# Kernel optimization log

Hardware: AMD Instinct MI355X
Metric: run time of the kernel (lower is better)

The kernel has to match this reference:

```python
import jax, jax.numpy as jnp
import numpy as np

N_NODES = 100000
N_EDGES = 1600000
IN_FEATS = 128
N_HIDDEN = 32
N_CLASSES = 47
HEADS = (4, 4)
NEG_SLOPE = 0.2


def setup_inputs() -> dict:
    key = jax.random.key(0)
    ks = jax.random.split(key, 12)
    x = jax.random.normal(ks[0], (N_NODES, IN_FEATS), dtype=jnp.float32)
    src = jax.random.randint(ks[1], (N_EDGES,), 0, N_NODES)
    dst = jax.random.randint(ks[2], (N_EDGES,), 0, N_NODES)
    inverse_idx = jax.random.randint(ks[3], (N_NODES,), 0, N_NODES)
    h1 = HEADS[0] * N_HIDDEN
    s1 = 1.0 / np.sqrt(IN_FEATS)
    W1 = jax.random.normal(ks[4], (IN_FEATS, h1), dtype=jnp.float32) * s1
    al1 = jax.random.normal(ks[5], (HEADS[0], N_HIDDEN), dtype=jnp.float32) * 0.1
    ar1 = jax.random.normal(ks[6], (HEADS[0], N_HIDDEN), dtype=jnp.float32) * 0.1
    b1 = jnp.zeros((h1,), dtype=jnp.float32)
    h2 = HEADS[1] * N_CLASSES
    s2 = 1.0 / np.sqrt(h1)
    W2 = jax.random.normal(ks[7], (h1, h2), dtype=jnp.float32) * s2
    al2 = jax.random.normal(ks[8], (HEADS[1], N_CLASSES), dtype=jnp.float32) * 0.1
    ar2 = jax.random.normal(ks[9], (HEADS[1], N_CLASSES), dtype=jnp.float32) * 0.1
    b2 = jnp.zeros((h2,), dtype=jnp.float32)
    return {"x": x, "src": src, "dst": dst, "inverse_idx": inverse_idx,
            "W1": W1, "al1": al1, "ar1": ar1, "b1": b1,
            "W2": W2, "al2": al2, "ar2": ar2, "b2": b2}


def gat_conv(h, src, dst, W, al, ar, b, heads, out_dim, apply_elu):
    # DGL GATConv (feat_drop=attn_drop=0, eval mode):
    # projected per-head features, edge attention, per-dst softmax, aggregate.
    feat = (h @ W).reshape(-1, heads, out_dim)               # (N, H, D)
    el = jnp.einsum('nhd,hd->nh', feat, al)                  # (N, H)
    er = jnp.einsum('nhd,hd->nh', feat, ar)                  # (N, H)
    e = el[src] + er[dst]                                    # (E, H)
    e = jnp.where(e > 0, e, NEG_SLOPE * e)                   # LeakyReLU
    m = jax.ops.segment_max(e, dst, num_segments=N_NODES)    # (N, H)
    m = jnp.where(jnp.isfinite(m), m, 0.0)
    ex = jnp.exp(e - m[dst])
    s = jax.ops.segment_sum(ex, dst, num_segments=N_NODES)   # (N, H)
    alpha = ex / jnp.maximum(s[dst], 1e-9)                   # (E, H)
    msg = feat[src] * alpha[:, :, None]                      # (E, H, D)
    out = jax.ops.segment_sum(msg, dst, num_segments=N_NODES)  # (N, H, D)
    out = out + b.reshape(1, heads, out_dim)
    if apply_elu:
        out = jax.nn.elu(out)
    return out


def reference(x, src, dst, inverse_idx, W1, al1, ar1, b1, W2, al2, ar2, b2):
    # Layer 0: GATConv + ELU, flatten heads, then NPFeatureShuffle reindex.
    h = gat_conv(x, src, dst, W1, al1, ar1, b1, HEADS[0], N_HIDDEN, True)
    h = h.reshape(N_NODES, HEADS[0] * N_HIDDEN)
    h = h[inverse_idx]  # cross-partition shuffle reindex
    # Layer 1: GATConv, no activation, mean over heads.
    h = gat_conv(h, src, dst, W2, al2, ar2, b2, HEADS[1], N_CLASSES, False)
    return h.mean(axis=1)  # (N, n_classes)
```

## Files before the change

### kernel.cpp

```cpp
#include <hip/hip_runtime.h>
#include <hip/hip_bf16.h>
#include <hip/hip_fp16.h>
#include <type_traits>

#define N_NODES 100000
#define N_EDGES 1600000

typedef _Float16 half8_t __attribute__((ext_vector_type(8)));
typedef _Float16 half4_t __attribute__((ext_vector_type(4)));
typedef float floatx4 __attribute__((ext_vector_type(4)));

__global__ void count_deg(const int* __restrict__ dst, int* __restrict__ deg, int E) {
    int i = blockIdx.x * blockDim.x + threadIdx.x;
    if (i < E) atomicAdd(&deg[dst[i]], 1);
}

__global__ void block_sums(const int* __restrict__ deg, int* __restrict__ bsum, int N) {
    __shared__ int ws[4];
    const int t = threadIdx.x;
    int i = blockIdx.x * 256 + t;
    int v = (i < N) ? deg[i] : 0;
    #pragma unroll
    for (int o = 32; o; o >>= 1) v += __shfl_down(v, o, 64);
    if ((t & 63) == 0) ws[t >> 6] = v;
    __syncthreads();
    if (t == 0) bsum[blockIdx.x] = ws[0] + ws[1] + ws[2] + ws[3];
}

__global__ void scan_bsum(int* __restrict__ bsum, int nb) {
    __shared__ int sh[512];
    const int t = threadIdx.x;
    sh[t] = (t < nb) ? bsum[t] : 0;
    __syncthreads();
    for (int o = 1; o < 512; o <<= 1) {
        int v = (t >= o) ? sh[t - o] : 0;
        __syncthreads();
        sh[t] += v;
        __syncthreads();
    }
    if (t < nb) bsum[t] = sh[t];
}

__global__ void scan_final(const int* __restrict__ deg, const int* __restrict__ bsum,
                           int* __restrict__ row_ptr, int* __restrict__ cursor,
                           int* __restrict__ csr_dst, int N) {
    __shared__ int ws[4];
    const int t = threadIdx.x;
    const int b = blockIdx.x;
    const int i = b * 256 + t;
    const int lane = t & 63;
    const int wid = t >> 6;
    int v = (i < N) ? deg[i] : 0;
    int x = v;
    #pragma unroll
    for (int o = 1; o < 64; o <<= 1) {
        int y = __shfl_up(x, o, 64);
        if (lane >= o) x += y;
    }
    if (lane == 63) ws[wid] = x;
    __syncthreads();
    int prefix = (b > 0) ? bsum[b - 1] : 0;
    for (int k = 0; k < wid; ++k) prefix += ws[k];
    if (i < N) {
        int st = prefix + x - v;
        row_ptr[i + 1] = prefix + x;
        cursor[i] = st;
        for (int j = 0; j < v; ++j) csr_dst[st + j] = i;
    }
    if (i == 0) row_ptr[0] = 0;
}

__global__ void scatter_edges_part(const int* __restrict__ src, const int* __restrict__ dst,
                                   int* __restrict__ cursor, int* __restrict__ e_src, int E) {
    const int part = blockIdx.x & 7;
    const int sb = blockIdx.x >> 3;
    const int nslices = gridDim.x >> 3;
    const int psz = N_NODES / 8;
    const int lo = part * psz;
    const int hi = (part == 7) ? N_NODES : lo + psz;
    const int begin = (int)((long long)E * sb / nslices);
    const int end = (int)((long long)E * (sb + 1) / nslices);
    for (int i = begin + threadIdx.x; i < end; i += blockDim.x) {
        int d = dst[i];
        if (d >= lo && d < hi) {
            int p = atomicAdd(&cursor[d], 1);
            e_src[p] = src[i];
        }
    }
}

__global__ void prep_w(const float* __restrict__ W1, const float* __restrict__ W2,
                       __half* __restrict__ Wt1, __half* __restrict__ Wt2) {
    const int c = blockIdx.x;
    const int k = threadIdx.x;
    if (c < 128) {
        Wt1[c * 128 + k] = __float2half(W1[k * 128 + c]);
    } else {
        int c2 = c - 128;
        float v = (c2 < 188) ? W2[k * 188 + c2] : 0.f;
        Wt2[c2 * 128 + k] = __float2half(v);
    }
}

template <int NTILES, int NLOG, int OSTRIDE, bool PADSTORE, bool GATHER, typename AT>
__global__ __launch_bounds__(256) void gemm_mfma(
    const AT* __restrict__ A, const __half* __restrict__ Wt,
    __half* __restrict__ C, const int* __restrict__ gather, int N) {
    constexpr int LDA = 136;
    __shared__ _Float16 As[64 * LDA];
    __shared__ int ridx[64];
    const int tid = threadIdx.x;
    const int r0 = blockIdx.x * 64;

    if (tid < 64) {
        int row = r0 + tid;
        int pr = 0;
        if (row < N) pr = GATHER ? gather[row] : row;
        ridx[tid] = pr;
    }
    __syncthreads();

    {
        const int r = tid >> 2, q = tid & 3;
        const int src = ridx[r];
        if constexpr (std::is_same<AT, float>::value) {
            const float4* A4 = (const float4*)A;
            #pragma unroll
            for (int i = 0; i < 8; ++i) {
                float4 v = A4[(size_t)src * 32 + q * 8 + i];
                half4_t hv = {(_Float16)v.x, (_Float16)v.y, (_Float16)v.z, (_Float16)v.w};
                *(half4_t*)&As[r * LDA + q * 32 + i * 4] = hv;
            }
        } else {
            const uint4* A4 = (const uint4*)A;
            #pragma unroll
            for (int i = 0; i < 4; ++i) {
                uint4 v = A4[(size_t)src * 16 + q * 4 + i];
                *(uint4*)&As[r * LDA + q * 32 + i * 8] = v;
            }
        }
    }
    __syncthreads();

    const int lane = tid & 63;
    const int wave = tid >> 6;
    const int col = lane & 15;
    const int quad = lane >> 4;
    const int arow = wave * 16 + col;

    floatx4 acc[NTILES];
    #pragma unroll
    for (int t = 0; t < NTILES; ++t) acc[t] = (floatx4){0.f, 0.f, 0.f, 0.f};

    #pragma unroll
    for (int kc = 0; kc < 4; ++kc) {
        half8_t a = *(const half8_t*)&As[arow * LDA + kc * 32 + quad * 8];
        #pragma unroll
        for (int t = 0; t < NTILES; ++t) {
            half8_t b = *(const half8_t*)&Wt[(size_t)(t * 16 + col) * 128 + kc * 32 + quad * 8];
            acc[t] = __builtin_amdgcn_mfma_f32_16x16x32_f16(a, b, acc[t], 0, 0, 0);
        }
    }

    #pragma unroll
    for (int t = 0; t < NTILES; ++t) {
        #pragma unroll
        for (int r = 0; r < 4; ++r) {
            int row = r0 + wave * 16 + quad * 4 + r;
            int c = t * 16 + col;
            if (row < N && c < NLOG) {
                int sc = PADSTORE ? (c + c / 47) : c;
                C[(size_t)row * OSTRIDE + sc] = __float2half(acc[t][r]);
            }
        }
    }
}

__global__ __launch_bounds__(256) void elr1_wave(
    const __half* __restrict__ feat, const float* __restrict__ al, const float* __restrict__ ar,
    float* __restrict__ el, float* __restrict__ er) {
    const int t = threadIdx.x;
    const int lane = t & 63;
    const int n = blockIdx.x * 4 + (t >> 6);
    const __half2* f2 = (const __half2*)feat;
    float2 g = __half22float2(f2[(size_t)n * 64 + lane]);
    float2 a = ((const float2*)al)[lane];
    float2 b = ((const float2*)ar)[lane];
    float sl = g.x * a.x + g.y * a.y;
    float sr = g.x * b.x + g.y * b.y;
    #pragma unroll
    for (int o = 1; o < 16; o <<= 1) {
        sl += __shfl_xor(sl, o, 64);
        sr += __shfl_xor(sr, o, 64);
    }
    if ((lane & 15) == 0) {
        int h = lane >> 4;
        el[n * 4 + h] = sl;
        er[n * 4 + h] = sr;
    }
}

__global__ __launch_bounds__(256) void elr2_wave(
    const __half* __restrict__ feat, const float* __restrict__ al, const float* __restrict__ ar,
    float* __restrict__ el, float* __restrict__ er) {
    const int t = threadIdx.x;
    const int lane = t & 63;
    const int n = blockIdx.x * 4 + (t >> 6);
    float sl = 0.f, sr = 0.f;
    int h = 0, q = 0;
    if (lane < 48) {
        h = lane / 12;
        q = lane - h * 12;
        const half4_t* f4 = (const half4_t*)feat;
        half4_t g = f4[(size_t)n * 48 + lane];
        const int d0 = q * 4;
        #pragma unroll
        for (int j = 0; j < 4; ++j) {
            int d = d0 + j;
            if (d < 47) {
                float gv = (float)g[j];
                sl = fmaf(gv, al[h * 47 + d], sl);
                sr = fmaf(gv, ar[h * 47 + d], sr);
            }
        }
    }
    sl += __shfl(sl, lane + 6, 64);
    sr += __shfl(sr, lane + 6, 64);
    sl += __shfl(sl, lane + 3, 64);
    sr += __shfl(sr, lane + 3, 64);
    float l1 = __shfl(sl, lane + 1, 64), l2 = __shfl(sl, lane + 2, 64);
    float r1 = __shfl(sr, lane + 1, 64), r2 = __shfl(sr, lane + 2, 64);
    sl += l1 + l2;
    sr += r1 + r2;
    if (lane < 48 && q == 0) {
        el[n * 4 + h] = sl;
        er[n * 4 + h] = sr;
    }
}

__global__ void edge_weights(const int* __restrict__ e_src, const int* __restrict__ csr_dst,
                             const float* __restrict__ el, const float* __restrict__ er,
                             __half* __restrict__ w, int E) {
    int i = blockIdx.x * blockDim.x + threadIdx.x;
    if (i >= E) return;
    int s = e_src[i], d = csr_dst[i];
    float4 a = ((const float4*)el)[s];
    float4 b = ((const float4*)er)[d];
    float e0 = a.x + b.x; e0 = (e0 > 0.f) ? e0 : 0.2f * e0;
    float e1 = a.y + b.y; e1 = (e1 > 0.f) ? e1 : 0.2f * e1;
    float e2 = a.z + b.z; e2 = (e2 > 0.f) ? e2 : 0.2f * e2;
    float e3 = a.w + b.w; e3 = (e3 > 0.f) ? e3 : 0.2f * e3;
    __half2* w2 = (__half2*)w;
    w2[i * 2 + 0] = __floats2half2_rn(__expf(e0), __expf(e1));
    w2[i * 2 + 1] = __floats2half2_rn(__expf(e2), __expf(e3));
}

__global__ __launch_bounds__(256) void gat_gather1(
    const __half* __restrict__ feat, const __half* __restrict__ w,
    const int* __restrict__ row_ptr, const int* __restrict__ e_src,
    const float* __restrict__ bias, __half* __restrict__ out) {
    const int t = threadIdx.x;
    const int lane = t & 63;
    const int n = blockIdx.x * 4 + (t >> 6);
    const int h = lane >> 4;
    const int start = row_ptr[n], end = row_ptr[n + 1];
    const __half2* f2 = (const __half2*)feat;
    float ax = 0.f, ay = 0.f, s = 0.f;
    int i = start;
    for (; i + 4 <= end; i += 4) {
        int sv0 = e_src[i + 0], sv1 = e_src[i + 1], sv2 = e_src[i + 2], sv3 = e_src[i + 3];
        float w0 = __half2float(w[(i + 0) * 4 + h]);
        float w1 = __half2float(w[(i + 1) * 4 + h]);
        float w2 = __half2float(w[(i + 2) * 4 + h]);
        float w3 = __half2float(w[(i + 3) * 4 + h]);
        __half2 f0 = f2[(size_t)sv0 * 64 + lane];
        __half2 f1 = f2[(size_t)sv1 * 64 + lane];
        __half2 f2v = f2[(size_t)sv2 * 64 + lane];
        __half2 f3 = f2[(size_t)sv3 * 64 + lane];
        float2 g0 = __half22float2(f0), g1 = __half22float2(f1);
        float2 g2 = __half22float2(f2v), g3 = __half22float2(f3);
        s += (w0 + w1) + (w2 + w3);
        ax += w0 * g0.x + w1 * g1.x + w2 * g2.x + w3 * g3.x;
        ay += w0 * g0.y + w1 * g1.y + w2 * g2.y + w3 * g3.y;
    }
    for (; i < end; ++i) {
        int sv = e_src[i];
        float ww = __half2float(w[i * 4 + h]);
        float2 g = __half22float2(f2[(size_t)sv * 64 + lane]);
        s += ww;
        ax += ww * g.x;
        ay += ww * g.y;
    }
    float inv = 1.f / fmaxf(s, 1e-9f);
    float ox = ax * inv + bias[lane * 2 + 0];
    float oy = ay * inv + bias[lane * 2 + 1];
    ox = (ox > 0.f) ? ox : (__expf(ox) - 1.f);
    oy = (oy > 0.f) ? oy : (__expf(oy) - 1.f);
    ((__half2*)out)[(size_t)n * 64 + lane] = __floats2half2_rn(ox, oy);
}

__global__ __launch_bounds__(256) void gat_gather2(
    const __half* __restrict__ feat, const __half* __restrict__ w,
    const int* __restrict__ row_ptr, const int* __restrict__ e_src,
    const float* __restrict__ bias, float* __restrict__ out) {
    const int t = threadIdx.x;
    const int lane = t & 63;
    const int n = blockIdx.x * 4 + (t >> 6);
    if (lane < 48) {
        const int h = lane / 12;
        const int q = lane - h * 12;
        const int start = row_ptr[n], end = row_ptr[n + 1];
        const half4_t* f4 = (const half4_t*)feat;
        float a0 = 0.f, a1 = 0.f, a2 = 0.f, a3 = 0.f, s = 0.f;
        int i = start;
        for (; i + 4 <= end; i += 4) {
            int sv0 = e_src[i + 0], sv1 = e_src[i + 1], sv2 = e_src[i + 2], sv3 = e_src[i + 3];
            float w0 = __half2float(w[(i + 0) * 4 + h]);
            float w1 = __half2float(w[(i + 1) * 4 + h]);
            float w2 = __half2float(w[(i + 2) * 4 + h]);
            float w3 = __half2float(w[(i + 3) * 4 + h]);
            half4_t f0 = f4[(size_t)sv0 * 48 + lane];
            half4_t f1 = f4[(size_t)sv1 * 48 + lane];
            half4_t f2 = f4[(size_t)sv2 * 48 + lane];
            half4_t f3 = f4[(size_t)sv3 * 48 + lane];
            s += (w0 + w1) + (w2 + w3);
            a0 += w0 * (float)f0[0] + w1 * (float)f1[0] + w2 * (float)f2[0] + w3 * (float)f3[0];
            a1 += w0 * (float)f0[1] + w1 * (float)f1[1] + w2 * (float)f2[1] + w3 * (float)f3[1];
            a2 += w0 * (float)f0[2] + w1 * (float)f1[2] + w2 * (float)f2[2] + w3 * (float)f3[2];
            a3 += w0 * (float)f0[3] + w1 * (float)f1[3] + w2 * (float)f2[3] + w3 * (float)f3[3];
        }
        for (; i < end; ++i) {
            int sv = e_src[i];
            float ww = __half2float(w[i * 4 + h]);
            half4_t f0 = f4[(size_t)sv * 48 + lane];
            s += ww;
            a0 += ww * (float)f0[0];
            a1 += ww * (float)f0[1];
            a2 += ww * (float)f0[2];
            a3 += ww * (float)f0[3];
        }
        if (q == 11) a3 = 0.f;
        float inv = 1.f / fmaxf(s, 1e-9f);
        const int d0 = q * 4;
        float b0 = bias[h * 47 + d0 + 0];
        float b1 = bias[h * 47 + d0 + 1];
        float b2 = bias[h * 47 + d0 + 2];
        float b3 = (d0 + 3 < 47) ? bias[h * 47 + d0 + 3] : 0.f;
        float r0 = a0 * inv + b0;
        float r1 = a1 * inv + b1;
        float r2 = a2 * inv + b2;
        float r3 = a3 * inv + b3;
        float t0 = r0 + __shfl(r0, lane + 12, 64) + __shfl(r0, lane + 24, 64) + __shfl(r0, lane + 36, 64);
        float t1 = r1 + __shfl(r1, lane + 12, 64) + __shfl(r1, lane + 24, 64) + __shfl(r1, lane + 36, 64);
        float t2 = r2 + __shfl(r2, lane + 12, 64) + __shfl(r2, lane + 24, 64) + __shfl(r2, lane + 36, 64);
        float t3 = r3 + __shfl(r3, lane + 12, 64) + __shfl(r3, lane + 24, 64) + __shfl(r3, lane + 36, 64);
        if (h == 0) {
            size_t base = (size_t)n * 47 + d0;
            out[base + 0] = 0.25f * t0;
            out[base + 1] = 0.25f * t1;
            out[base + 2] = 0.25f * t2;
            if (d0 + 3 < 47) out[base + 3] = 0.25f * t3;
        }
    }
}

extern "C" void kernel_launch(void* const* d_in, const int* in_sizes, int n_in,
                              void* d_out, int out_size, void* d_ws, size_t ws_size,
                              hipStream_t stream) {
    const int N = N_NODES, E = N_EDGES;
    const float* x    = (const float*)d_in[0];
    const int*   src  = (const int*)d_in[1];
    const int*   dst  = (const int*)d_in[2];
    const int*   inv  = (const int*)d_in[3];
    const float* W1   = (const float*)d_in[4];
    const float* al1  = (const float*)d_in[5];
    const float* ar1  = (const float*)d_in[6];
    const float* b1   = (const float*)d_in[7];
    const float* W2   = (const float*)d_in[8];
    const float* al2  = (const float*)d_in[9];
    const float* ar2  = (const float*)d_in[10];
    const float* b2   = (const float*)d_in[11];
    float* out = (float*)d_out;

    char* p = (char*)d_ws;
    auto carve = [&](size_t bytes) {
        char* q = p;
        p += (bytes + 255) & ~size_t(255);
        return q;
    };
    __half* feat1   = (__half*)carve((size_t)N * 128 * 2);
    __half* feat2   = (__half*)carve((size_t)N * 192 * 2);
    __half* hbuf    = (__half*)carve((size_t)N * 128 * 2);
    __half* Wt1     = (__half*)carve(128 * 128 * 2);
    __half* Wt2     = (__half*)carve(192 * 128 * 2);
    float*  el      = (float*)carve((size_t)N * 4 * 4);
    float*  er      = (float*)carve((size_t)N * 4 * 4);
    int*    deg     = (int*)carve((size_t)N * 4);
    int*    row_ptr = (int*)carve((size_t)(N + 1) * 4);
    int*    cursor  = (int*)carve((size_t)N * 4);
    int*    bsum    = (int*)carve(512 * 4);
    int*    e_src   = (int*)carve((size_t)E * 4);
    int*    csr_dst = (int*)carve((size_t)E * 4);
    __half* ew      = (__half*)carve((size_t)E * 4 * 2);

    const int nb = (N + 255) / 256;

    hipMemsetAsync(deg, 0, (size_t)N * 4, stream);
    count_deg<<<(E + 255) / 256, 256, 0, stream>>>(dst, deg, E);
    block_sums<<<nb, 256, 0, stream>>>(deg, bsum, N);
    scan_bsum<<<1, 512, 0, stream>>>(bsum, nb);
    scan_final<<<nb, 256, 0, stream>>>(deg, bsum, row_ptr, cursor, csr_dst, N);
    scatter_edges_part<<<2048, 256, 0, stream>>>(src, dst, cursor, e_src, E);

    prep_w<<<320, 128, 0, stream>>>(W1, W2, Wt1, Wt2);

    gemm_mfma<8, 128, 128, false, false, float><<<(N + 63) / 64, 256, 0, stream>>>(x, Wt1, feat1, nullptr, N);
    elr1_wave<<<(N + 3) / 4, 256, 0, stream>>>(feat1, al1, ar1, el, er);
    edge_weights<<<(E + 255) / 256, 256, 0, stream>>>(e_src, csr_dst, el, er, ew, E);
    gat_gather1<<<(N + 3) / 4, 256, 0, stream>>>(feat1, ew, row_ptr, e_src, b1, hbuf);

    gemm_mfma<12, 188, 192, true, true, __half><<<(N + 63) / 64, 256, 0, stream>>>(hbuf, Wt2, feat2, inv, N);
    elr2_wave<<<(N + 3) / 4, 256, 0, stream>>>(feat2, al2, ar2, el, er);
    edge_weights<<<(E + 255) / 256, 256, 0, stream>>>(e_src, csr_dst, el, er, ew, E);
    gat_gather2<<<(N + 3) / 4, 256, 0, stream>>>(feat2, ew, row_ptr, e_src, b2, out);
}
```

Before: 581.6 us.

## Fold attention vectors into GEMM weights and compute edge weights inside gather

Precomputes W·al and W·ar as extra weight columns so the GEMM emits el/er directly, removing the separate elr kernels. Edge softmax numerators are now computed on the fly in the gather kernels from el[src]+er[dst], eliminating the edge_weights kernels, the ew buffer and the csr_dst array along with its serial fill loop in scan_final. This removes several launches and about 1.6M-edge-sized reads and writes per layer, at the cost of an extra random el load plus exp per edge per lane in the gathers and slightly different rounding because el/er now come from fp16-rounded folded weights.

```diff
diff --git a/kernel.cpp b/kernel.cpp
--- a/kernel.cpp
+++ b/kernel.cpp
@@ -42,8 +42,7 @@
 }
 
 __global__ void scan_final(const int* __restrict__ deg, const int* __restrict__ bsum,
-                           int* __restrict__ row_ptr, int* __restrict__ cursor,
-                           int* __restrict__ csr_dst, int N) {
+                           int* __restrict__ row_ptr, int* __restrict__ cursor, int N) {
     __shared__ int ws[4];
     const int t = threadIdx.x;
     const int b = blockIdx.x;
@@ -62,10 +61,8 @@
     int prefix = (b > 0) ? bsum[b - 1] : 0;
     for (int k = 0; k < wid; ++k) prefix += ws[k];
     if (i < N) {
-        int st = prefix + x - v;
         row_ptr[i + 1] = prefix + x;
-        cursor[i] = st;
-        for (int j = 0; j < v; ++j) csr_dst[st + j] = i;
+        cursor[i] = prefix + x - v;
     }
     if (i == 0) row_ptr[0] = 0;
 }
@@ -90,22 +87,45 @@
 }
 
 __global__ void prep_w(const float* __restrict__ W1, const float* __restrict__ W2,
+                       const float* __restrict__ al1, const float* __restrict__ ar1,
+                       const float* __restrict__ al2, const float* __restrict__ ar2,
                        __half* __restrict__ Wt1, __half* __restrict__ Wt2) {
     const int c = blockIdx.x;
     const int k = threadIdx.x;
     if (c < 128) {
         Wt1[c * 128 + k] = __float2half(W1[k * 128 + c]);
-    } else {
-        int c2 = c - 128;
+    } else if (c < 144) {
+        int j = c - 128;
+        float v = 0.f;
+        if (j < 8) {
+            int h = j & 3;
+            const float* a = (j < 4) ? al1 : ar1;
+            for (int d = 0; d < 32; ++d)
+                v = fmaf(W1[k * 128 + h * 32 + d], a[h * 32 + d], v);
+        }
+        Wt1[c * 128 + k] = __float2half(v);
+    } else if (c < 336) {
+        int c2 = c - 144;
         float v = (c2 < 188) ? W2[k * 188 + c2] : 0.f;
         Wt2[c2 * 128 + k] = __float2half(v);
-    }
-}
-
-template <int NTILES, int NLOG, int OSTRIDE, bool PADSTORE, bool GATHER, typename AT>
+    } else {
+        int j = c - 336;
+        float v = 0.f;
+        if (j < 8) {
+            int h = j & 3;
+            const float* a = (j < 4) ? al2 : ar2;
+            for (int d = 0; d < 47; ++d)
+                v = fmaf(W2[k * 188 + h * 47 + d], a[h * 47 + d], v);
+        }
+        Wt2[(192 + j) * 128 + k] = __float2half(v);
+    }
+}
+
+template <int TT, int NLOG, int OSTRIDE, bool PADSTORE, bool GATHER, typename AT>
 __global__ __launch_bounds__(256) void gemm_mfma(
     const AT* __restrict__ A, const __half* __restrict__ Wt,
-    __half* __restrict__ C, const int* __restrict__ gather, int N) {
+    __half* __restrict__ C, float* __restrict__ el, float* __restrict__ er,
+    const int* __restrict__ gather, int N) {
     constexpr int LDA = 136;
     __shared__ _Float16 As[64 * LDA];
     __shared__ int ridx[64];
@@ -148,22 +168,22 @@
     const int quad = lane >> 4;
     const int arow = wave * 16 + col;
 
-    floatx4 acc[NTILES];
-    #pragma unroll
-    for (int t = 0; t < NTILES; ++t) acc[t] = (floatx4){0.f, 0.f, 0.f, 0.f};
+    floatx4 acc[TT];
+    #pragma unroll
+    for (int t = 0; t < TT; ++t) acc[t] = (floatx4){0.f, 0.f, 0.f, 0.f};
 
     #pragma unroll
     for (int kc = 0; kc < 4; ++kc) {
         half8_t a = *(const half8_t*)&As[arow * LDA + kc * 32 + quad * 8];
         #pragma unroll
-        for (int t = 0; t < NTILES; ++t) {
+        for (int t = 0; t < TT; ++t) {
             half8_t b = *(const half8_t*)&Wt[(size_t)(t * 16 + col) * 128 + kc * 32 + quad * 8];
             acc[t] = __builtin_amdgcn_mfma_f32_16x16x32_f16(a, b, acc[t], 0, 0, 0);
         }
     }
 
     #pragma unroll
-    for (int t = 0; t < NTILES; ++t) {
+    for (int t = 0; t < TT - 1; ++t) {
         #pragma unroll
         for (int r = 0; r < 4; ++r) {
             int row = r0 + wave * 16 + quad * 4 + r;
@@ -174,89 +194,19 @@
             }
         }
     }
-}
-
-__global__ __launch_bounds__(256) void elr1_wave(
-    const __half* __restrict__ feat, const float* __restrict__ al, const float* __restrict__ ar,
-    float* __restrict__ el, float* __restrict__ er) {
-    const int t = threadIdx.x;
-    const int lane = t & 63;
-    const int n = blockIdx.x * 4 + (t >> 6);
-    const __half2* f2 = (const __half2*)feat;
-    float2 g = __half22float2(f2[(size_t)n * 64 + lane]);
-    float2 a = ((const float2*)al)[lane];
-    float2 b = ((const float2*)ar)[lane];
-    float sl = g.x * a.x + g.y * a.y;
-    float sr = g.x * b.x + g.y * b.y;
-    #pragma unroll
-    for (int o = 1; o < 16; o <<= 1) {
-        sl += __shfl_xor(sl, o, 64);
-        sr += __shfl_xor(sr, o, 64);
-    }
-    if ((lane & 15) == 0) {
-        int h = lane >> 4;
-        el[n * 4 + h] = sl;
-        er[n * 4 + h] = sr;
-    }
-}
-
-__global__ __launch_bounds__(256) void elr2_wave(
-    const __half* __restrict__ feat, const float* __restrict__ al, const float* __restrict__ ar,
-    float* __restrict__ el, float* __restrict__ er) {
-    const int t = threadIdx.x;
-    const int lane = t & 63;
-    const int n = blockIdx.x * 4 + (t >> 6);
-    float sl = 0.f, sr = 0.f;
-    int h = 0, q = 0;
-    if (lane < 48) {
-        h = lane / 12;
-        q = lane - h * 12;
-        const half4_t* f4 = (const half4_t*)feat;
-        half4_t g = f4[(size_t)n * 48 + lane];
-        const int d0 = q * 4;
-        #pragma unroll
-        for (int j = 0; j < 4; ++j) {
-            int d = d0 + j;
-            if (d < 47) {
-                float gv = (float)g[j];
-                sl = fmaf(gv, al[h * 47 + d], sl);
-                sr = fmaf(gv, ar[h * 47 + d], sr);
-            }
-        }
-    }
-    sl += __shfl(sl, lane + 6, 64);
-    sr += __shfl(sr, lane + 6, 64);
-    sl += __shfl(sl, lane + 3, 64);
-    sr += __shfl(sr, lane + 3, 64);
-    float l1 = __shfl(sl, lane + 1, 64), l2 = __shfl(sl, lane + 2, 64);
-    float r1 = __shfl(sr, lane + 1, 64), r2 = __shfl(sr, lane + 2, 64);
-    sl += l1 + l2;
-    sr += r1 + r2;
-    if (lane < 48 && q == 0) {
-        el[n * 4 + h] = sl;
-        er[n * 4 + h] = sr;
-    }
-}
-
-__global__ void edge_weights(const int* __restrict__ e_src, const int* __restrict__ csr_dst,
-                             const float* __restrict__ el, const float* __restrict__ er,
-                             __half* __restrict__ w, int E) {
-    int i = blockIdx.x * blockDim.x + threadIdx.x;
-    if (i >= E) return;
-    int s = e_src[i], d = csr_dst[i];
-    float4 a = ((const float4*)el)[s];
-    float4 b = ((const float4*)er)[d];
-    float e0 = a.x + b.x; e0 = (e0 > 0.f) ? e0 : 0.2f * e0;
-    float e1 = a.y + b.y; e1 = (e1 > 0.f) ? e1 : 0.2f * e1;
-    float e2 = a.z + b.z; e2 = (e2 > 0.f) ? e2 : 0.2f * e2;
-    float e3 = a.w + b.w; e3 = (e3 > 0.f) ? e3 : 0.2f * e3;
-    __half2* w2 = (__half2*)w;
-    w2[i * 2 + 0] = __floats2half2_rn(__expf(e0), __expf(e1));
-    w2[i * 2 + 1] = __floats2half2_rn(__expf(e2), __expf(e3));
+    #pragma unroll
+    for (int r = 0; r < 4; ++r) {
+        int row = r0 + wave * 16 + quad * 4 + r;
+        if (row < N) {
+            if (col < 4) el[row * 4 + col] = acc[TT - 1][r];
+            else if (col < 8) er[row * 4 + (col - 4)] = acc[TT - 1][r];
+        }
+    }
 }
 
 __global__ __launch_bounds__(256) void gat_gather1(
-    const __half* __restrict__ feat, const __half* __restrict__ w,
+    const __half* __restrict__ feat, const float* __restrict__ el,
+    const float* __restrict__ er,
     const int* __restrict__ row_ptr, const int* __restrict__ e_src,
     const float* __restrict__ bias, __half* __restrict__ out) {
     const int t = threadIdx.x;
@@ -265,14 +215,19 @@
     const int h = lane >> 4;
     const int start = row_ptr[n], end = row_ptr[n + 1];
     const __half2* f2 = (const __half2*)feat;
+    const float ern = er[n * 4 + h];
     float ax = 0.f, ay = 0.f, s = 0.f;
     int i = start;
     for (; i + 4 <= end; i += 4) {
         int sv0 = e_src[i + 0], sv1 = e_src[i + 1], sv2 = e_src[i + 2], sv3 = e_src[i + 3];
-        float w0 = __half2float(w[(i + 0) * 4 + h]);
-        float w1 = __half2float(w[(i + 1) * 4 + h]);
-        float w2 = __half2float(w[(i + 2) * 4 + h]);
-        float w3 = __half2float(w[(i + 3) * 4 + h]);
+        float e0 = el[sv0 * 4 + h] + ern;
+        float e1 = el[sv1 * 4 + h] + ern;
+        float e2 = el[sv2 * 4 + h] + ern;
+        float e3 = el[sv3 * 4 + h] + ern;
+        float w0 = __expf(fmaxf(e0, 0.2f * e0));
+        float w1 = __expf(fmaxf(e1, 0.2f * e1));
+        float w2 = __expf(fmaxf(e2, 0.2f * e2));
+        float w3 = __expf(fmaxf(e3, 0.2f * e3));
         __half2 f0 = f2[(size_t)sv0 * 64 + lane];
         __half2 f1 = f2[(size_t)sv1 * 64 + lane];
         __half2 f2v = f2[(size_t)sv2 * 64 + lane];
@@ -285,7 +240,8 @@
     }
     for (; i < end; ++i) {
         int sv = e_src[i];
-        float ww = __half2float(w[i * 4 + h]);
+        float e = el[sv * 4 + h] + ern;
+        float ww = __expf(fmaxf(e, 0.2f * e));
         float2 g = __half22float2(f2[(size_t)sv * 64 + lane]);
         s += ww;
         ax += ww * g.x;
@@ -300,7 +256,8 @@
 }
 
 __global__ __launch_bounds__(256) void gat_gather2(
-    const __half* __restrict__ feat, const __half* __restrict__ w,
+    const __half* __restrict__ feat, const float* __restrict__ el,
+    const float* __restrict__ er,
     const int* __restrict__ row_ptr, const int* __restrict__ e_src,
     const float* __restrict__ bias, float* __restrict__ out) {
     const int t = threadIdx.x;
@@ -311,14 +268,19 @@
         const int q = lane - h * 12;
         const int start = row_ptr[n], end = row_ptr[n + 1];
         const half4_t* f4 = (const half4_t*)feat;
+        const float ern = er[n * 4 + h];
         float a0 = 0.f, a1 = 0.f, a2 = 0.f, a3 = 0.f, s = 0.f;
         int i = start;
         for (; i + 4 <= end; i += 4) {
             int sv0 = e_src[i + 0], sv1 = e_src[i + 1], sv2 = e_src[i + 2], sv3 = e_src[i + 3];
-            float w0 = __half2float(w[(i + 0) * 4 + h]);
-            float w1 = __half2float(w[(i + 1) * 4 + h]);
-            float w2 = __half2float(w[(i + 2) * 4 + h]);
-            float w3 = __half2float(w[(i + 3) * 4 + h]);
+            float e0 = el[sv0 * 4 + h] + ern;
+            float e1 = el[sv1 * 4 + h] + ern;
+            float e2 = el[sv2 * 4 + h] + ern;
+            float e3 = el[sv3 * 4 + h] + ern;
+            float w0 = __expf(fmaxf(e0, 0.2f * e0));
+            float w1 = __expf(fmaxf(e1, 0.2f * e1));
+            float w2 = __expf(fmaxf(e2, 0.2f * e2));
+            float w3 = __expf(fmaxf(e3, 0.2f * e3));
             half4_t f0 = f4[(size_t)sv0 * 48 + lane];
             half4_t f1 = f4[(size_t)sv1 * 48 + lane];
             half4_t f2 = f4[(size_t)sv2 * 48 + lane];
@@ -331,7 +293,8 @@
         }
         for (; i < end; ++i) {
             int sv = e_src[i];
-            float ww = __half2float(w[i * 4 + h]);
+            float e = el[sv * 4 + h] + ern;
+            float ww = __expf(fmaxf(e, 0.2f * e));
             half4_t f0 = f4[(size_t)sv * 48 + lane];
             s += ww;
             a0 += ww * (float)f0[0];
@@ -391,8 +354,8 @@
     __half* feat1   = (__half*)carve((size_t)N * 128 * 2);
     __half* feat2   = (__half*)carve((size_t)N * 192 * 2);
     __half* hbuf    = (__half*)carve((size_t)N * 128 * 2);
-    __half* Wt1     = (__half*)carve(128 * 128 * 2);
-    __half* Wt2     = (__half*)carve(192 * 128 * 2);
+    __half* Wt1     = (__half*)carve(144 * 128 * 2);
+    __half* Wt2     = (__half*)carve(208 * 128 * 2);
     float*  el      = (float*)carve((size_t)N * 4 * 4);
     float*  er      = (float*)carve((size_t)N * 4 * 4);
     int*    deg     = (int*)carve((size_t)N * 4);
@@ -400,8 +363,6 @@
     int*    cursor  = (int*)carve((size_t)N * 4);
     int*    bsum    = (int*)carve(512 * 4);
     int*    e_src   = (int*)carve((size_t)E * 4);
-    int*    csr_dst = (int*)carve((size_t)E * 4);
-    __half* ew      = (__half*)carve((size_t)E * 4 * 2);
 
     const int nb = (N + 255) / 256;
 
@@ -409,18 +370,16 @@
     count_deg<<<(E + 255) / 256, 256, 0, stream>>>(dst, deg, E);
     block_sums<<<nb, 256, 0, stream>>>(deg, bsum, N);
     scan_bsum<<<1, 512, 0, stream>>>(bsum, nb);
-    scan_final<<<nb, 256, 0, stream>>>(deg, bsum, row_ptr, cursor, csr_dst, N);
+    scan_final<<<nb, 256, 0, stream>>>(deg, bsum, row_ptr, cursor, N);
     scatter_edges_part<<<2048, 256, 0, stream>>>(src, dst, cursor, e_src, E);
 
-    prep_w<<<320, 128, 0, stream>>>(W1, W2, Wt1, Wt2);
-
-    gemm_mfma<8, 128, 128, false, false, float><<<(N + 63) / 64, 256, 0, stream>>>(x, Wt1, feat1, nullptr, N);
-    elr1_wave<<<(N + 3) / 4, 256, 0, stream>>>(feat1, al1, ar1, el, er);
-    edge_weights<<<(E + 255) / 256, 256, 0, stream>>>(e_src, csr_dst, el, er, ew, E);
-    gat_gather1<<<(N + 3) / 4, 256, 0, stream>>>(feat1, ew, row_ptr, e_src, b1, hbuf);
-
-    gemm_mfma<12, 188, 192, true, true, __half><<<(N + 63) / 64, 256, 0, stream>>>(hbuf, Wt2, feat2, inv, N);
-    elr2_wave<<<(N + 3) / 4, 256, 0, stream>>>(feat2, al2, ar2, el, er);
-    edge_weights<<<(E + 255) / 256, 256, 0, stream>>>(e_src, csr_dst, el, er, ew, E);
-    gat_gather2<<<(N + 3) / 4, 256, 0, stream>>>(feat2, ew, row_ptr, e_src, b2, out);
-}
+    prep_w<<<352, 128, 0, stream>>>(W1, W2, al1, ar1, al2, ar2, Wt1, Wt2);
+
+    gemm_mfma<9, 128, 128, false, false, float><<<(N + 63) / 64, 256, 0, stream>>>(
+        x, Wt1, feat1, el, er, nullptr, N);
+    gat_gather1<<<(N + 3) / 4, 256, 0, stream>>>(feat1, el, er, row_ptr, e_src, b1, hbuf);
+
+    gemm_mfma<13, 188, 192, true, true, __half><<<(N + 63) / 64, 256, 0, stream>>>(
+        hbuf, Wt2, feat2, el, er, inv, N);
+    gat_gather2<<<(N + 3) / 4, 256, 0, stream>>>(feat2, el, er, row_ptr, e_src, b2, out);
+}
```

New measurement: 532.4 us. 8.5% less time.
